# Optimization experiments

Measured on AMD Instinct MI355X. Metric: run time of the kernel, lower is better.

## Reference

```python
import jax, jax.numpy as jnp
import numpy as np

B, S, H = 32, 4096, 512

def setup_inputs() -> dict:
    key = jax.random.key(0)
    k1, k2, k3, k4, k5 = jax.random.split(key, 5)
    scale = 1.0 / np.sqrt(H)
    return {
        "query": jax.random.normal(k1, (B, 1, H), dtype=jnp.float32),
        "keys": jax.random.normal(k2, (B, S, H), dtype=jnp.float32),
        "Wa": jax.random.normal(k3, (H, H), dtype=jnp.float32) * scale,
        "Ua": jax.random.normal(k4, (H, H), dtype=jnp.float32) * scale,
        "Va": jax.random.normal(k5, (H, 1), dtype=jnp.float32) * scale,
    }

def reference(query, keys, Wa, Ua, Va):
    # additive (Bahdanau) attention scores: Va^T tanh(Wa q + Ua k)
    q_proj = jnp.einsum('bqh,hd->bqd', query, Wa)          # [B,1,H]
    k_proj = jnp.einsum('bsh,hd->bsd', keys, Ua)           # [B,S,H]
    scores = jnp.einsum('bsd,d->bs', jnp.tanh(q_proj + k_proj), Va[:, 0])  # [B,S]
    weights = jax.nn.softmax(scores, axis=-1)[:, None, :]  # [B,1,S]
    context = jnp.einsum('bqs,bsh->bqh', weights, keys)    # [B,1,H]
    return (context, weights)
```

## Files before the change

kernel.cpp:

```cpp
#include <hip/hip_runtime.h>
#include <hip/hip_bf16.h>

#define B_ 32
#define S_ 4096
#define H_ 512

typedef short bf16x8 __attribute__((ext_vector_type(8)));
typedef float f32x4 __attribute__((ext_vector_type(4)));

__device__ inline unsigned short f2bf(float x) {
    unsigned u = __float_as_uint(x);
    return (unsigned short)((u + 0x7fffu + ((u >> 16) & 1u)) >> 16);
}

__device__ inline float fast_tanh(float x) {
    float e = __expf(2.f * x);
    return 1.f - 2.f / (e + 1.f);
}

__global__ void k_prep_ua(const float* __restrict__ Ua,
                          unsigned short* __restrict__ ua_tiled) {
    __shared__ float tile[32][33];
    int h0 = blockIdx.x * 32, d0 = blockIdx.y * 32;
    int tx = threadIdx.x, ty = threadIdx.y;
#pragma unroll
    for (int j = 0; j < 4; ++j)
        tile[ty + j * 8][tx] = Ua[(size_t)(h0 + ty + j * 8) * H_ + d0 + tx];
    __syncthreads();
#pragma unroll
    for (int j = 0; j < 4; ++j) {
        int dd = ty + j * 8;
        ua_tiled[((size_t)blockIdx.x * H_ + d0 + dd) * 32 + tx] = f2bf(tile[tx][dd]);
    }
}

__global__ __launch_bounds__(512) void k_qproj(const float* __restrict__ query,
                                               const float* __restrict__ Wa,
                                               float* __restrict__ qproj) {
    __shared__ float q[H_];
    int b = blockIdx.x, d = threadIdx.x;
    q[d] = query[(size_t)b * H_ + d];
    __syncthreads();
    float acc = 0.f;
    for (int h = 0; h < H_; ++h)
        acc = fmaf(q[h], Wa[(size_t)h * H_ + d], acc);
    qproj[(size_t)b * H_ + d] = acc;
}

#define BM  64
#define BK  32
#define LDT 40

__global__ __launch_bounds__(512) void k_scores(
    const float* __restrict__ keys, const unsigned short* __restrict__ ua_tiled,
    const float* __restrict__ qproj, const float* __restrict__ Va,
    float* __restrict__ scores) {
    __shared__ unsigned short As[BM * LDT];
    __shared__ unsigned short Bs[H_ * LDT];
    __shared__ float sm_part[8][BM];

    int tid = threadIdx.x;
    int wave = tid >> 6, lane = tid & 63;
    int wn = wave;
    int lq = lane & 15, lh = lane >> 4;
    int b = blockIdx.y;
    int m0 = blockIdx.x * BM;

    const float* keysb = keys + (size_t)b * S_ * H_;

    f32x4 acc[4][4];
#pragma unroll
    for (int i = 0; i < 4; ++i)
#pragma unroll
        for (int j = 0; j < 4; ++j) acc[i][j] = (f32x4){0.f, 0.f, 0.f, 0.f};

    int ar = tid >> 3, ac4 = (tid & 7) << 2;
    const float* aptr = keysb + (size_t)(m0 + ar) * H_ + ac4;
    const unsigned short* bptr = ua_tiled + (size_t)tid * 32;

    for (int kk = 0; kk < H_ / BK; ++kk) {
        int k0 = kk * BK;
        float4 av = *(const float4*)(aptr + k0);
        const unsigned short* bsrc = bptr + (size_t)kk * H_ * 32;
        uint4 bv0 = *(const uint4*)(bsrc + 0);
        uint4 bv1 = *(const uint4*)(bsrc + 8);
        uint4 bv2 = *(const uint4*)(bsrc + 16);
        uint4 bv3 = *(const uint4*)(bsrc + 24);
        __syncthreads();
        ushort4 aw;
        aw.x = f2bf(av.x); aw.y = f2bf(av.y); aw.z = f2bf(av.z); aw.w = f2bf(av.w);
        *(ushort4*)&As[ar * LDT + ac4] = aw;
        *(uint4*)&Bs[tid * LDT + 0]  = bv0;
        *(uint4*)&Bs[tid * LDT + 8]  = bv1;
        *(uint4*)&Bs[tid * LDT + 16] = bv2;
        *(uint4*)&Bs[tid * LDT + 24] = bv3;
        __syncthreads();

        bf16x8 af[4], bfr[4];
#pragma unroll
        for (int mf = 0; mf < 4; ++mf)
            af[mf] = *(const bf16x8*)&As[(mf * 16 + lq) * LDT + lh * 8];
#pragma unroll
        for (int nf = 0; nf < 4; ++nf)
            bfr[nf] = *(const bf16x8*)&Bs[(wn * 64 + nf * 16 + lq) * LDT + lh * 8];
#pragma unroll
        for (int mf = 0; mf < 4; ++mf)
#pragma unroll
            for (int nf = 0; nf < 4; ++nf)
                acc[mf][nf] = __builtin_amdgcn_mfma_f32_16x16x32_bf16(
                    af[mf], bfr[nf], acc[mf][nf], 0, 0, 0);
    }

    float va_r[4], qp_r[4];
#pragma unroll
    for (int nf = 0; nf < 4; ++nf) {
        int n = wn * 64 + nf * 16 + lq;
        va_r[nf] = Va[n];
        qp_r[nf] = qproj[(size_t)b * H_ + n];
    }
#pragma unroll
    for (int mf = 0; mf < 4; ++mf) {
#pragma unroll
        for (int reg = 0; reg < 4; ++reg) {
            float p = 0.f;
#pragma unroll
            for (int nf = 0; nf < 4; ++nf)
                p += va_r[nf] * fast_tanh(qp_r[nf] + acc[mf][nf][reg]);
            p += __shfl_xor(p, 1);
            p += __shfl_xor(p, 2);
            p += __shfl_xor(p, 4);
            p += __shfl_xor(p, 8);
            if (lq == 0) sm_part[wn][mf * 16 + lh * 4 + reg] = p;
        }
    }
    __syncthreads();
    if (tid < BM) {
        float s = 0.f;
#pragma unroll
        for (int w = 0; w < 8; ++w) s += sm_part[w][tid];
        scores[(size_t)b * S_ + m0 + tid] = s;
    }
}

__global__ __launch_bounds__(512) void k_softmax(float* __restrict__ wts) {
    __shared__ float red[8];
    int b = blockIdx.x, tid = threadIdx.x;
    float* row = wts + (size_t)b * S_;
    float v[8];
    float m = -1e30f;
#pragma unroll
    for (int i = 0; i < 8; ++i) {
        v[i] = row[tid + i * 512];
        m = fmaxf(m, v[i]);
    }
#pragma unroll
    for (int o = 1; o < 64; o <<= 1) m = fmaxf(m, __shfl_xor(m, o));
    if ((tid & 63) == 0) red[tid >> 6] = m;
    __syncthreads();
    m = red[0];
#pragma unroll
    for (int w = 1; w < 8; ++w) m = fmaxf(m, red[w]);
    float sum = 0.f;
#pragma unroll
    for (int i = 0; i < 8; ++i) {
        v[i] = __expf(v[i] - m);
        sum += v[i];
    }
#pragma unroll
    for (int o = 1; o < 64; o <<= 1) sum += __shfl_xor(sum, o);
    __syncthreads();
    if ((tid & 63) == 0) red[tid >> 6] = sum;
    __syncthreads();
    float tot = 0.f;
#pragma unroll
    for (int w = 0; w < 8; ++w) tot += red[w];
    float inv = 1.f / tot;
#pragma unroll
    for (int i = 0; i < 8; ++i) row[tid + i * 512] = v[i] * inv;
}

__global__ __launch_bounds__(512) void k_ctx_part(const float* __restrict__ keys,
                                                  const float* __restrict__ wts,
                                                  float* __restrict__ part) {
    int c = blockIdx.x, b = blockIdx.y, h = threadIdx.x;
    const float* wrow = wts + (size_t)b * S_ + c * 256;
    const float* kbase = keys + ((size_t)b * S_ + c * 256) * H_ + h;
    float acc = 0.f;
#pragma unroll 8
    for (int s = 0; s < 256; ++s)
        acc = fmaf(wrow[s], kbase[(size_t)s * H_], acc);
    part[((size_t)c * B_ + b) * H_ + h] = acc;
}

__global__ __launch_bounds__(512) void k_ctx_reduce(const float* __restrict__ part,
                                                    float* __restrict__ ctx) {
    int b = blockIdx.x, h = threadIdx.x;
    float s = 0.f;
#pragma unroll
    for (int c = 0; c < 16; ++c) s += part[((size_t)c * B_ + b) * H_ + h];
    ctx[(size_t)b * H_ + h] = s;
}

extern "C" void kernel_launch(void* const* d_in, const int* in_sizes, int n_in,
                              void* d_out, int out_size, void* d_ws, size_t ws_size,
                              hipStream_t stream) {
    const float* query = (const float*)d_in[0];
    const float* keys  = (const float*)d_in[1];
    const float* Wa    = (const float*)d_in[2];
    const float* Ua    = (const float*)d_in[3];
    const float* Va    = (const float*)d_in[4];

    float* out = (float*)d_out;
    float* ctx = out;
    float* wts = out + B_ * H_;

    char* ws = (char*)d_ws;
    unsigned short* ua_tiled = (unsigned short*)ws;
    float* qproj = (float*)(ws + 524288);
    float* part  = (float*)(ws + 524288 + 65536);

    k_prep_ua<<<dim3(16, 16), dim3(32, 8), 0, stream>>>(Ua, ua_tiled);
    k_qproj<<<dim3(32), dim3(512), 0, stream>>>(query, Wa, qproj);
    k_scores<<<dim3(64, 32), dim3(512), 0, stream>>>(keys, ua_tiled, qproj, Va, wts);
    k_softmax<<<dim3(32), dim3(512), 0, stream>>>(wts);
    k_ctx_part<<<dim3(16, 32), dim3(512), 0, stream>>>(keys, wts, part);
    k_ctx_reduce<<<dim3(32), dim3(512), 0, stream>>>(part, ctx);
}
```

Measured before the change: 200.6 us.

## Retile score GEMM over N blocks with swizzled LDS, direct-to-LDS loads, prefetch

The scores kernel now tiles 128 rows by 128 output columns per block, with a grid over N blocks, and uses XOR-swizzled LDS layouts. Ua tiles are copied straight into LDS with global_load_lds, and the next keys chunk is prefetched into registers. Partial scores per N block are written to a workspace and summed inside softmax. The context reduction is also split into more chunks for more parallelism. Keys are now read four times, once per N block, in exchange for smaller LDS use, higher occupancy and fewer bank conflicts.

```diff
diff --git a/kernel.cpp b/kernel.cpp
--- a/kernel.cpp
+++ b/kernel.cpp
@@ -6,6 +6,7 @@
 #define H_ 512
 
 typedef short bf16x8 __attribute__((ext_vector_type(8)));
+typedef unsigned short u16x8 __attribute__((ext_vector_type(8)));
 typedef float f32x4 __attribute__((ext_vector_type(4)));
 
 __device__ inline unsigned short f2bf(float x) {
@@ -18,8 +19,18 @@
     return 1.f - 2.f / (e + 1.f);
 }
 
+__device__ __forceinline__ void stage16(const void* g, void* lds_base, int lane) {
+#if defined(__has_builtin) && __has_builtin(__builtin_amdgcn_global_load_lds)
+    __builtin_amdgcn_global_load_lds(
+        (const __attribute__((address_space(1))) unsigned char*)g,
+        (__attribute__((address_space(3))) unsigned char*)lds_base, 16, 0, 0);
+#else
+    ((uint4*)lds_base)[lane] = *(const uint4*)g;
+#endif
+}
+
 __global__ void k_prep_ua(const float* __restrict__ Ua,
-                          unsigned short* __restrict__ ua_tiled) {
+                          unsigned short* __restrict__ ua_t) {
     __shared__ float tile[32][33];
     int h0 = blockIdx.x * 32, d0 = blockIdx.y * 32;
     int tx = threadIdx.x, ty = threadIdx.y;
@@ -29,8 +40,8 @@
     __syncthreads();
 #pragma unroll
     for (int j = 0; j < 4; ++j) {
-        int dd = ty + j * 8;
-        ua_tiled[((size_t)blockIdx.x * H_ + d0 + dd) * 32 + tx] = f2bf(tile[tx][dd]);
+        int dl = ty + j * 8;
+        ua_t[(size_t)(d0 + dl) * H_ + h0 + tx] = f2bf(tile[tx][dl]);
     }
 }
 
@@ -47,74 +58,93 @@
     qproj[(size_t)b * H_ + d] = acc;
 }
 
-#define BM  64
-#define BK  32
-#define LDT 40
-
-__global__ __launch_bounds__(512) void k_scores(
-    const float* __restrict__ keys, const unsigned short* __restrict__ ua_tiled,
+__global__ __launch_bounds__(512, 4) void k_scores(
+    const float* __restrict__ keys, const unsigned short* __restrict__ ua_t,
     const float* __restrict__ qproj, const float* __restrict__ Va,
-    float* __restrict__ scores) {
-    __shared__ unsigned short As[BM * LDT];
-    __shared__ unsigned short Bs[H_ * LDT];
-    __shared__ float sm_part[8][BM];
+    float* __restrict__ part_sc) {
+    __shared__ __align__(16) unsigned char As[16384];
+    __shared__ __align__(16) unsigned char Bs[16384];
+    __shared__ float smp[4][128];
 
     int tid = threadIdx.x;
     int wave = tid >> 6, lane = tid & 63;
-    int wn = wave;
     int lq = lane & 15, lh = lane >> 4;
-    int b = blockIdx.y;
-    int m0 = blockIdx.x * BM;
+    int wm = wave >> 2;
+    int wnn = wave & 3;
+    int b = blockIdx.z, nb = blockIdx.y, m0 = blockIdx.x * 128;
 
     const float* keysb = keys + (size_t)b * S_ * H_;
 
-    f32x4 acc[4][4];
+    int r = tid >> 2, qtr = tid & 3;
+    const float* aptr = keysb + (size_t)(m0 + r) * H_ + qtr * 16;
+    unsigned aswz = (unsigned)((r & 7) << 4);
+    unsigned abase = (unsigned)(r * 128);
+
+    int rb0 = wave * 8 + (lane >> 3);
+    int rb1 = 64 + rb0;
+    unsigned cb = (unsigned)((lane & 7) * 16);
+    const unsigned char* uab = (const unsigned char*)ua_t;
+    const unsigned char* bsrc0 = uab + ((size_t)(nb * 128 + rb0)) * 1024 + (cb ^ ((rb0 & 7) << 4));
+    const unsigned char* bsrc1 = uab + ((size_t)(nb * 128 + rb1)) * 1024 + (cb ^ ((rb1 & 7) << 4));
+    unsigned char* ldsB0 = Bs + wave * 1024;
+    unsigned char* ldsB1 = Bs + 8192 + wave * 1024;
+
+    f32x4 acc[4][2];
 #pragma unroll
     for (int i = 0; i < 4; ++i)
 #pragma unroll
-        for (int j = 0; j < 4; ++j) acc[i][j] = (f32x4){0.f, 0.f, 0.f, 0.f};
-
-    int ar = tid >> 3, ac4 = (tid & 7) << 2;
-    const float* aptr = keysb + (size_t)(m0 + ar) * H_ + ac4;
-    const unsigned short* bptr = ua_tiled + (size_t)tid * 32;
-
-    for (int kk = 0; kk < H_ / BK; ++kk) {
-        int k0 = kk * BK;
-        float4 av = *(const float4*)(aptr + k0);
-        const unsigned short* bsrc = bptr + (size_t)kk * H_ * 32;
-        uint4 bv0 = *(const uint4*)(bsrc + 0);
-        uint4 bv1 = *(const uint4*)(bsrc + 8);
-        uint4 bv2 = *(const uint4*)(bsrc + 16);
-        uint4 bv3 = *(const uint4*)(bsrc + 24);
+        for (int j = 0; j < 2; ++j) acc[i][j] = (f32x4){0.f, 0.f, 0.f, 0.f};
+
+    unsigned swzR = (unsigned)((lq & 7) << 4);
+
+    float4 ar[2][4];
+#pragma unroll
+    for (int j = 0; j < 4; ++j) ar[0][j] = *(const float4*)(aptr + j * 4);
+
+#pragma unroll
+    for (int t = 0; t < 8; ++t) {
+        const int cur = t & 1, nxt = cur ^ 1;
         __syncthreads();
-        ushort4 aw;
-        aw.x = f2bf(av.x); aw.y = f2bf(av.y); aw.z = f2bf(av.z); aw.w = f2bf(av.w);
-        *(ushort4*)&As[ar * LDT + ac4] = aw;
-        *(uint4*)&Bs[tid * LDT + 0]  = bv0;
-        *(uint4*)&Bs[tid * LDT + 8]  = bv1;
-        *(uint4*)&Bs[tid * LDT + 16] = bv2;
-        *(uint4*)&Bs[tid * LDT + 24] = bv3;
+        if (t < 7) {
+#pragma unroll
+            for (int j = 0; j < 4; ++j)
+                ar[nxt][j] = *(const float4*)(aptr + (t + 1) * 64 + j * 4);
+        }
+        stage16(bsrc0 + t * 128, ldsB0, lane);
+        stage16(bsrc1 + t * 128, ldsB1, lane);
+#pragma unroll
+        for (int j16 = 0; j16 < 2; ++j16) {
+            float4 x = ar[cur][2 * j16], y = ar[cur][2 * j16 + 1];
+            u16x8 v;
+            v[0] = f2bf(x.x); v[1] = f2bf(x.y); v[2] = f2bf(x.z); v[3] = f2bf(x.w);
+            v[4] = f2bf(y.x); v[5] = f2bf(y.y); v[6] = f2bf(y.z); v[7] = f2bf(y.w);
+            *(u16x8*)(As + abase + ((unsigned)(qtr * 32 + j16 * 16) ^ aswz)) = v;
+        }
         __syncthreads();
 
-        bf16x8 af[4], bfr[4];
-#pragma unroll
-        for (int mf = 0; mf < 4; ++mf)
-            af[mf] = *(const bf16x8*)&As[(mf * 16 + lq) * LDT + lh * 8];
-#pragma unroll
-        for (int nf = 0; nf < 4; ++nf)
-            bfr[nf] = *(const bf16x8*)&Bs[(wn * 64 + nf * 16 + lq) * LDT + lh * 8];
-#pragma unroll
-        for (int mf = 0; mf < 4; ++mf)
-#pragma unroll
-            for (int nf = 0; nf < 4; ++nf)
-                acc[mf][nf] = __builtin_amdgcn_mfma_f32_16x16x32_bf16(
-                    af[mf], bfr[nf], acc[mf][nf], 0, 0, 0);
-    }
-
-    float va_r[4], qp_r[4];
-#pragma unroll
-    for (int nf = 0; nf < 4; ++nf) {
-        int n = wn * 64 + nf * 16 + lq;
+#pragma unroll
+        for (int ks = 0; ks < 2; ++ks) {
+            bf16x8 af[4], bv[2];
+            unsigned koff = (unsigned)(ks * 64 + lh * 16) ^ swzR;
+#pragma unroll
+            for (int mf = 0; mf < 4; ++mf)
+                af[mf] = *(const bf16x8*)(As + (unsigned)((wm * 64 + mf * 16 + lq) * 128) + koff);
+#pragma unroll
+            for (int nf = 0; nf < 2; ++nf)
+                bv[nf] = *(const bf16x8*)(Bs + (unsigned)((wnn * 32 + nf * 16 + lq) * 128) + koff);
+#pragma unroll
+            for (int mf = 0; mf < 4; ++mf)
+#pragma unroll
+                for (int nf = 0; nf < 2; ++nf)
+                    acc[mf][nf] = __builtin_amdgcn_mfma_f32_16x16x32_bf16(
+                        af[mf], bv[nf], acc[mf][nf], 0, 0, 0);
+        }
+    }
+
+    float va_r[2], qp_r[2];
+#pragma unroll
+    for (int nf = 0; nf < 2; ++nf) {
+        int n = nb * 128 + wnn * 32 + nf * 16 + lq;
         va_r[nf] = Va[n];
         qp_r[nf] = qproj[(size_t)b * H_ + n];
     }
@@ -122,35 +152,36 @@
     for (int mf = 0; mf < 4; ++mf) {
 #pragma unroll
         for (int reg = 0; reg < 4; ++reg) {
-            float p = 0.f;
-#pragma unroll
-            for (int nf = 0; nf < 4; ++nf)
-                p += va_r[nf] * fast_tanh(qp_r[nf] + acc[mf][nf][reg]);
+            float p = va_r[0] * fast_tanh(qp_r[0] + acc[mf][0][reg])
+                    + va_r[1] * fast_tanh(qp_r[1] + acc[mf][1][reg]);
             p += __shfl_xor(p, 1);
             p += __shfl_xor(p, 2);
             p += __shfl_xor(p, 4);
             p += __shfl_xor(p, 8);
-            if (lq == 0) sm_part[wn][mf * 16 + lh * 4 + reg] = p;
-        }
-    }
-    __syncthreads();
-    if (tid < BM) {
-        float s = 0.f;
-#pragma unroll
-        for (int w = 0; w < 8; ++w) s += sm_part[w][tid];
-        scores[(size_t)b * S_ + m0 + tid] = s;
-    }
-}
-
-__global__ __launch_bounds__(512) void k_softmax(float* __restrict__ wts) {
+            if (lq == 0) smp[wnn][wm * 64 + mf * 16 + lh * 4 + reg] = p;
+        }
+    }
+    __syncthreads();
+    if (tid < 128) {
+        float s = smp[0][tid] + smp[1][tid] + smp[2][tid] + smp[3][tid];
+        part_sc[((size_t)nb * B_ + b) * S_ + m0 + tid] = s;
+    }
+}
+
+__global__ __launch_bounds__(512) void k_softmax(const float* __restrict__ part_sc,
+                                                 float* __restrict__ wts) {
     __shared__ float red[8];
     int b = blockIdx.x, tid = threadIdx.x;
-    float* row = wts + (size_t)b * S_;
+    const float* p0 = part_sc + (size_t)b * S_;
+    const float* p1 = p0 + (size_t)B_ * S_;
+    const float* p2 = p1 + (size_t)B_ * S_;
+    const float* p3 = p2 + (size_t)B_ * S_;
     float v[8];
     float m = -1e30f;
 #pragma unroll
     for (int i = 0; i < 8; ++i) {
-        v[i] = row[tid + i * 512];
+        int s = tid + i * 512;
+        v[i] = ((p0[s] + p1[s]) + (p2[s] + p3[s]));
         m = fmaxf(m, v[i]);
     }
 #pragma unroll
@@ -176,18 +207,18 @@
     for (int w = 0; w < 8; ++w) tot += red[w];
     float inv = 1.f / tot;
 #pragma unroll
-    for (int i = 0; i < 8; ++i) row[tid + i * 512] = v[i] * inv;
+    for (int i = 0; i < 8; ++i) wts[(size_t)b * S_ + tid + i * 512] = v[i] * inv;
 }
 
 __global__ __launch_bounds__(512) void k_ctx_part(const float* __restrict__ keys,
                                                   const float* __restrict__ wts,
                                                   float* __restrict__ part) {
     int c = blockIdx.x, b = blockIdx.y, h = threadIdx.x;
-    const float* wrow = wts + (size_t)b * S_ + c * 256;
-    const float* kbase = keys + ((size_t)b * S_ + c * 256) * H_ + h;
+    const float* wrow = wts + (size_t)b * S_ + c * 128;
+    const float* kbase = keys + ((size_t)b * S_ + c * 128) * H_ + h;
     float acc = 0.f;
 #pragma unroll 8
-    for (int s = 0; s < 256; ++s)
+    for (int s = 0; s < 128; ++s)
         acc = fmaf(wrow[s], kbase[(size_t)s * H_], acc);
     part[((size_t)c * B_ + b) * H_ + h] = acc;
 }
@@ -197,7 +228,7 @@
     int b = blockIdx.x, h = threadIdx.x;
     float s = 0.f;
 #pragma unroll
-    for (int c = 0; c < 16; ++c) s += part[((size_t)c * B_ + b) * H_ + h];
+    for (int c = 0; c < 32; ++c) s += part[((size_t)c * B_ + b) * H_ + h];
     ctx[(size_t)b * H_ + h] = s;
 }
 
@@ -215,14 +246,15 @@
     float* wts = out + B_ * H_;
 
     char* ws = (char*)d_ws;
-    unsigned short* ua_tiled = (unsigned short*)ws;
-    float* qproj = (float*)(ws + 524288);
-    float* part  = (float*)(ws + 524288 + 65536);
-
-    k_prep_ua<<<dim3(16, 16), dim3(32, 8), 0, stream>>>(Ua, ua_tiled);
+    unsigned short* ua_t = (unsigned short*)ws;
+    float* qproj   = (float*)(ws + 524288);
+    float* part_sc = (float*)(ws + 524288 + 65536);
+    float* part_cx = (float*)(ws + 524288 + 65536 + 2097152);
+
+    k_prep_ua<<<dim3(16, 16), dim3(32, 8), 0, stream>>>(Ua, ua_t);
     k_qproj<<<dim3(32), dim3(512), 0, stream>>>(query, Wa, qproj);
-    k_scores<<<dim3(64, 32), dim3(512), 0, stream>>>(keys, ua_tiled, qproj, Va, wts);
-    k_softmax<<<dim3(32), dim3(512), 0, stream>>>(wts);
-    k_ctx_part<<<dim3(16, 32), dim3(512), 0, stream>>>(keys, wts, part);
-    k_ctx_reduce<<<dim3(32), dim3(512), 0, stream>>>(part, ctx);
-}
+    k_scores<<<dim3(32, 4, 32), dim3(512), 0, stream>>>(keys, ua_t, qproj, Va, part_sc);
+    k_softmax<<<dim3(32), dim3(512), 0, stream>>>(part_sc, wts);
+    k_ctx_part<<<dim3(32, 32), dim3(512), 0, stream>>>(keys, wts, part_cx);
+    k_ctx_reduce<<<dim3(32), dim3(512), 0, stream>>>(part_cx, ctx);
+}
```

Result: slower. 218.8 us (+9.1%).
